# Kernel optimization log

Measured on AMD Instinct MI355X. Metric: run time of the kernel, lower is better.

Reference implementation:

```python
import jax, jax.numpy as jnp
import numpy as np

J = 17  # coco joints
SKEL = ((1, 2), (0, 1), (0, 2), (2, 4), (1, 3), (6, 8), (8, 10), (5, 7), (7, 9),
        (12, 14), (14, 16), (11, 13), (13, 15), (5, 6), (11, 12), (5, 11), (6, 12), (3, 5), (4, 6))
EPS = 1e-5


def make_adj():
    a = np.eye(J, dtype=np.float32)
    for i, j in SKEL:
        a[i, j] = 1.0
        a[j, i] = 1.0
    return jnp.asarray(a)


def conv_block(feat, W, b, g, be, adj):
    # feat: [B,V,Din], W: [V,Din,Dout], b/g/be: [V,Dout]
    h = jnp.einsum('bvd,vdo->bvo', feat, W) + b
    # BatchNorm1d (training mode): per-vertex, per-channel batch stats (biased var)
    mu = h.mean(axis=0)
    var = h.var(axis=0)
    h = (h - mu) * jax.lax.rsqrt(var + EPS) * g + be
    h = jnp.einsum('vu,buo->bvo', adj, h)  # adjacency aggregation
    return jax.nn.relu(h)


def setup_inputs() -> dict:
    key = jax.random.key(0)
    ks = jax.random.split(key, 10)
    B, Din = 8192, 2048
    s0 = 1.0 / np.sqrt(Din)
    s1 = 1.0 / np.sqrt(J)
    img_feat = jax.random.normal(ks[0], (B, J, Din), dtype=jnp.float32)
    # first GraphConvBlock: 2048 -> 17, per-vertex params
    W0 = jax.random.uniform(ks[1], (J, Din, J), jnp.float32, -s0, s0)
    b0 = jax.random.uniform(ks[2], (J, J), jnp.float32, -s0, s0)
    g0 = jnp.ones((J, J), jnp.float32)
    be0 = jnp.zeros((J, J), jnp.float32)
    # 4 GraphResBlocks x 2 GraphConvBlocks = 8 blocks of dim 17 -> 17
    Wr = jax.random.uniform(ks[3], (8, J, J, J), jnp.float32, -s1, s1)
    br = jax.random.uniform(ks[4], (8, J, J), jnp.float32, -s1, s1)
    gr = jnp.ones((8, J, J), jnp.float32)
    ber = jnp.zeros((8, J, J), jnp.float32)
    return {"img_feat": img_feat, "W0": W0, "b0": b0, "g0": g0, "be0": be0,
            "Wr": Wr, "br": br, "gr": gr, "ber": ber}


def reference(img_feat, W0, b0, g0, be0, Wr, br, gr, ber):
    adj = make_adj()
    feat = conv_block(img_feat, W0, b0, g0, be0, adj)  # [B,17,17]
    for r in range(4):  # 4 GraphResBlocks
        i0, i1 = 2 * r, 2 * r + 1
        h = conv_block(feat, Wr[i0], br[i0], gr[i0], ber[i0], adj)
        h = conv_block(h, Wr[i1], br[i1], gr[i1], ber[i1], adj)
        feat = h + feat  # residual
    return feat
```

## Files before the change

### kernel.cpp

```cpp
#include <hip/hip_runtime.h>

#define J 17
#define JP 18
#define VO 289
#define NB 8192
#define DIN 2048
#define EPSB 1e-5f
#define KC 512
#define RT 32
#define NCH 68

typedef __attribute__((ext_vector_type(8))) short bf16x8;
typedef __attribute__((ext_vector_type(4))) float f32x4;
typedef __attribute__((ext_vector_type(4))) float f32x4v;

__device__ __constant__ unsigned ADJM[J] = {
  0x7u, 0xFu, 0x17u, 0x2Au, 0x54u, 0x8E8u, 0x1170u, 0x2A0u, 0x540u,
  0x280u, 0x500u, 0x3820u, 0x5840u, 0xA800u, 0x15000u, 0xA000u, 0x14000u};

__device__ inline unsigned short f2bf(float x){
  unsigned u = __float_as_uint(x);
  return (unsigned short)((u + 0x7fffu + ((u>>16)&1u)) >> 16);
}

__global__ void zero_stats(float* p, int n) {
  int i = blockIdx.x*blockDim.x + threadIdx.x;
  int stride = gridDim.x*blockDim.x;
  for (; i < n; i += stride) p[i] = 0.f;
}

__global__ __launch_bounds__(256) void wconv_kernel(
    const float* __restrict__ W0, unsigned short* __restrict__ Wp)
{
  int t = blockIdx.x*256 + threadIdx.x;
  int v = t >> 11, k = t & 2047;
  const float* src = W0 + (size_t)t*J;
  unsigned short* dst = Wp + (((size_t)v*256 + (k>>3))*17)*8 + (k&7);
  #pragma unroll
  for (int o=0;o<J;++o)  dst[o*8] = f2bf(src[o]);
}

__global__ __launch_bounds__(256) void wfrag_kernel(
    const float* __restrict__ Wr, unsigned short* __restrict__ WfA,
    unsigned short* __restrict__ WfB)
{
  int t = blockIdx.x*256 + threadIdx.x;
  if (t < 8*17*64) {
    int s = t/(17*64), rem = t - s*17*64, v = rem>>6, ll = rem&63;
    int c = ll&15, o8 = ll>>4;
    unsigned short* dst = WfA + (size_t)t*8;
    const float* w = Wr + ((size_t)(s*J + v)*J)*J;
    #pragma unroll
    for (int j=0;j<8;++j){ int d=o8*8+j; dst[j] = (d<J) ? f2bf(w[(size_t)d*J + c]) : (unsigned short)0; }
  }
  if (t < 8*17*4) {
    int s = t/(17*4), rem = t - s*17*4, v = rem>>2, o8 = rem&3;
    unsigned short* dst = WfB + (size_t)t*8;
    const float* w = Wr + ((size_t)(s*J + v)*J)*J;
    #pragma unroll
    for (int j=0;j<8;++j){ int d=o8*8+j; dst[j] = (d<J) ? f2bf(w[(size_t)d*J + 16]) : (unsigned short)0; }
  }
}

__global__ __launch_bounds__(512) void conv0_kernel(
    const float* __restrict__ feat, const unsigned short* __restrict__ Wp,
    const float* __restrict__ b0, float* __restrict__ C,
    float* __restrict__ stat0)
{
  const int tid = threadIdx.x, w = tid>>6, l = tid&63;
  const int lo = l&15, oc = l>>4;
  const int sr = tid>>4, sc = tid&15;
  const int rowBase = blockIdx.x*RT;

  __shared__ __align__(16) unsigned short Ab[2][RT*KC];
  __shared__ float red[8][2][256];
  __shared__ float bS[VO], bQ[VO];

  for (int i=tid;i<VO;i+=512){ bS[i]=0.f; bQ[i]=0.f; }

  f32x4 acc00 = (f32x4){0.f,0.f,0.f,0.f};
  f32x4 acc01 = (f32x4){0.f,0.f,0.f,0.f};
  f32x4 acc10 = (f32x4){0.f,0.f,0.f,0.f};
  f32x4 acc11 = (f32x4){0.f,0.f,0.f,0.f};

  const float* frow = feat + (size_t)(rowBase + sr)*(J*DIN);
  f32x4v ld[8];

  auto issue = [&](int c){
    const f32x4v* src = (const f32x4v*)(frow + c*KC + sc*4);
    #pragma unroll
    for (int i=0;i<8;++i) ld[i] = __builtin_nontemporal_load(src + i*16);
  };
  auto writeLDS = [&](int buf){
    #pragma unroll
    for (int i=0;i<8;++i){
      ushort4 hv;
      hv.x=f2bf(ld[i].x); hv.y=f2bf(ld[i].y); hv.z=f2bf(ld[i].z); hv.w=f2bf(ld[i].w);
      const int f = sc*4 + i*64;
      *(ushort4*)&Ab[buf][(sr*KC + f) ^ ((sr&7)<<3)] = hv;
    }
  };

  issue(0); writeLDS(0);
  __syncthreads();

  const int swz = (lo&7)<<3;

  for (int c=0;c<NCH;++c){
    const int buf = c&1;
    if (c+1<NCH) issue(c+1);
    const int v = c>>2;
    #pragma unroll
    for (int ks=0;ks<2;++ks){
      const int kl = w*64 + ks*32 + oc*8;
      bf16x8 a0 = *(const bf16x8*)&Ab[buf][(lo*KC + kl) ^ swz];
      bf16x8 a1 = *(const bf16x8*)&Ab[buf][((16+lo)*KC + kl) ^ swz];
      const int kg8 = ((c&3)*KC + kl) >> 3;
      const unsigned short* fragBase = Wp + (((size_t)v*256 + kg8)*17)*8;
      bf16x8 bA = *(const bf16x8*)(fragBase + lo*8);
      bf16x8 bB = {0,0,0,0,0,0,0,0};
      if (lo==0) bB = *(const bf16x8*)(fragBase + 16*8);
      acc00 = __builtin_amdgcn_mfma_f32_16x16x32_bf16(a0, bA, acc00, 0,0,0);
      acc10 = __builtin_amdgcn_mfma_f32_16x16x32_bf16(a1, bA, acc10, 0,0,0);
      acc01 = __builtin_amdgcn_mfma_f32_16x16x32_bf16(a0, bB, acc01, 0,0,0);
      acc11 = __builtin_amdgcn_mfma_f32_16x16x32_bf16(a1, bB, acc11, 0,0,0);
    }
    if ((c&3)==3){
      #pragma unroll
      for (int pass=0; pass<2; ++pass){
        #pragma unroll
        for (int r=0;r<4;++r){
          red[w][0][(oc*4+r)*16+lo] = pass ? acc10[r] : acc00[r];
          red[w][1][(oc*4+r)*16+lo] = pass ? acc11[r] : acc01[r];
        }
        __syncthreads();
        if (tid < 256){
          const int er = tid>>4, ec = tid&15;
          const int ri = er*16+ec;
          float h0 = red[0][0][ri]+red[1][0][ri]+red[2][0][ri]+red[3][0][ri]
                   + red[4][0][ri]+red[5][0][ri]+red[6][0][ri]+red[7][0][ri]
                   + b0[v*J+ec];
          const int row = rowBase + pass*16 + er;
          C[(size_t)row*VO + v*J + ec] = h0;
          float s0 = h0, q0 = h0*h0;
          float s1 = 0.f, q1 = 0.f;
          if (ec==0){
            const int r2 = er*16;
            float h1 = red[0][1][r2]+red[1][1][r2]+red[2][1][r2]+red[3][1][r2]
                     + red[4][1][r2]+red[5][1][r2]+red[6][1][r2]+red[7][1][r2]
                     + b0[v*J+16];
            C[(size_t)row*VO + v*J + 16] = h1;
            s1 = h1; q1 = h1*h1;
          }
          s0 += __shfl_xor(s0,16); s0 += __shfl_xor(s0,32);
          q0 += __shfl_xor(q0,16); q0 += __shfl_xor(q0,32);
          s1 += __shfl_xor(s1,16); s1 += __shfl_xor(s1,32);
          q1 += __shfl_xor(q1,16); q1 += __shfl_xor(q1,32);
          if (l < 16){ atomicAdd(&bS[v*J+l], s0); atomicAdd(&bQ[v*J+l], q0); }
          if (l == 0){ atomicAdd(&bS[v*J+16], s1); atomicAdd(&bQ[v*J+16], q1); }
        }
        __syncthreads();
      }
      acc00 = (f32x4){0.f,0.f,0.f,0.f};
      acc01 = (f32x4){0.f,0.f,0.f,0.f};
      acc10 = (f32x4){0.f,0.f,0.f,0.f};
      acc11 = (f32x4){0.f,0.f,0.f,0.f};
    }
    if (c+1<NCH){
      writeLDS(buf^1);
      __syncthreads();
    }
  }

  __syncthreads();
  const int rep = blockIdx.x & 7;
  for (int i=tid;i<VO;i+=512){
    atomicAdd(&stat0[rep*512+i],        bS[i]);
    atomicAdd(&stat0[4096 + rep*512+i], bQ[i]);
  }
}

template<int RESID,int WRITEF,int CONV>
__global__ __launch_bounds__(256) void chain_kernel(
  const float* __restrict__ Cin, float* __restrict__ Cout,
  float* __restrict__ F,
  const float* __restrict__ statJ,
  const float* __restrict__ g, const float* __restrict__ be,
  const unsigned short* __restrict__ wfA_g, const unsigned short* __restrict__ wfB_g,
  const float* __restrict__ bc,
  float* __restrict__ statN)
{
  __shared__ float aC[VO], cC[VO], bb[VO];
  __shared__ float ssum[VO], ssq[VO];
  __shared__ float hb1[4][4][J*JP];
  __shared__ __align__(16) unsigned short hb2[16*576];

  const int tid = threadIdx.x, wv = tid>>6, lane = tid&63;
  const int lo = lane&15, oc = lane>>4;
  const int rowBase = blockIdx.x*16;

  for (int i=tid;i<VO;i+=256){
    float s=0.f,q=0.f;
    #pragma unroll
    for (int r=0;r<8;++r){ s += statJ[r*512+i]; q += statJ[4096 + r*512+i]; }
    float mu  = s*(1.f/NB);
    float var = q*(1.f/NB) - mu*mu;
    float A = rsqrtf(var + EPSB)*g[i];
    aC[i]=A; cC[i]=be[i]-mu*A;
    ssum[i]=0.f; ssq[i]=0.f;
    if (CONV) bb[i]=bc[i];
  }
  if (CONV){
    for (int i=tid;i<16*576/8;i+=256) ((uint4*)hb2)[i] = (uint4){0,0,0,0};
  }
  __syncthreads();

  #pragma unroll
  for (int r4=0;r4<4;++r4){
    const int row = wv*4 + r4;
    const float* cr = Cin + (size_t)(rowBase+row)*VO;
    #pragma unroll
    for (int s=0;s<5;++s){
      int vo = lane + 64*s;
      if (vo<VO){ int vtx=vo/J, o=vo-vtx*J; hb1[wv][r4][vtx*JP+o] = cr[vo]*aC[vo] + cC[vo]; }
    }
  }
  asm volatile("s_waitcnt lgkmcnt(0)" ::: "memory");
  #pragma unroll
  for (int r4=0;r4<4;++r4){
    const int row = wv*4 + r4;
    #pragma unroll
    for (int s=0;s<5;++s){
      int vo = lane + 64*s;
      if (vo<VO){
        int vtx=vo/J, o=vo-vtx*J;
        unsigned m = ADJM[vtx];
        float a = 0.f;
        while (m){ int u=__ffs(m)-1; m&=m-1; a += hb1[wv][r4][u*JP+o]; }
        a = a>0.f ? a : 0.f;
        size_t gi = (size_t)(rowBase+row)*VO + vo;
        if (RESID)  a += F[gi];
        if (WRITEF) F[gi] = a;
        if (CONV){
          int idx = (row*576 + vtx*32 + o) ^ ((row&7)<<3);
          hb2[idx] = f2bf(a);
        } else {
          Cout[gi] = a;
        }
      }
    }
  }
  if (!CONV) return;
  __syncthreads();

  for (int v=wv; v<J; v+=4){
    const int aidx = (lo*576 + v*32 + oc*8) ^ ((lo&7)<<3);
    bf16x8 a  = *(const bf16x8*)&hb2[aidx];
    bf16x8 bA = *(const bf16x8*)(wfA_g + ((size_t)v*64 + lane)*8);
    bf16x8 bB = {0,0,0,0,0,0,0,0};
    if (lo==0) bB = *(const bf16x8*)(wfB_g + ((size_t)v*4 + oc)*8);
    f32x4 acc0 = (f32x4){0.f,0.f,0.f,0.f};
    f32x4 acc1 = (f32x4){0.f,0.f,0.f,0.f};
    acc0 = __builtin_amdgcn_mfma_f32_16x16x32_bf16(a, bA, acc0, 0,0,0);
    acc1 = __builtin_amdgcn_mfma_f32_16x16x32_bf16(a, bB, acc1, 0,0,0);

    const float bias0 = bb[v*J+lo];
    const float bias1 = bb[v*J+16];
    float s0=0.f,q0=0.f,s1=0.f,q1=0.f;
    #pragma unroll
    for (int r=0;r<4;++r){
      const int row = rowBase + oc*4 + r;
      const float h0 = acc0[r] + bias0;
      Cout[(size_t)row*VO + v*J + lo] = h0;
      s0 += h0; q0 += h0*h0;
      if (lo==0){
        const float h1 = acc1[r] + bias1;
        Cout[(size_t)row*VO + v*J + 16] = h1;
        s1 += h1; q1 += h1*h1;
      }
    }
    s0 += __shfl_xor(s0,16); s0 += __shfl_xor(s0,32);
    q0 += __shfl_xor(q0,16); q0 += __shfl_xor(q0,32);
    s1 += __shfl_xor(s1,16); s1 += __shfl_xor(s1,32);
    q1 += __shfl_xor(q1,16); q1 += __shfl_xor(q1,32);
    if (lane < 16){ atomicAdd(&ssum[v*J+lo], s0); atomicAdd(&ssq[v*J+lo], q0); }
    if (lane == 0){ atomicAdd(&ssum[v*J+16], s1); atomicAdd(&ssq[v*J+16], q1); }
  }
  __syncthreads();
  const int rep = blockIdx.x & 7;
  for (int i=tid;i<VO;i+=256){
    atomicAdd(&statN[rep*512+i],        ssum[i]);
    atomicAdd(&statN[4096 + rep*512+i], ssq[i]);
  }
}

extern "C" void kernel_launch(void* const* d_in, const int* in_sizes, int n_in,
                              void* d_out, int out_size, void* d_ws, size_t ws_size,
                              hipStream_t stream)
{
  (void)in_sizes; (void)n_in; (void)out_size; (void)ws_size;
  const float* img = (const float*)d_in[0];
  const float* W0  = (const float*)d_in[1];
  const float* b0  = (const float*)d_in[2];
  const float* g0  = (const float*)d_in[3];
  const float* be0 = (const float*)d_in[4];
  const float* Wr  = (const float*)d_in[5];
  const float* br  = (const float*)d_in[6];
  const float* gr  = (const float*)d_in[7];
  const float* ber = (const float*)d_in[8];

  float* ws = (float*)d_ws;
  float* ST = ws;
  unsigned short* Wp  = (unsigned short*)(ws + 73728);
  unsigned short* WfA = (unsigned short*)(ws + 73728 + 300000);
  unsigned short* WfB = WfA + 8*17*64*8;
  float* Ca = ws + 73728 + 300000 + 40000;
  float* Cb = Ca + (size_t)NB*VO;
  float* F  = Cb + (size_t)NB*VO;
  float* out = (float*)d_out;

  zero_stats<<<72,256,0,stream>>>(ST, 9*8192);
  wconv_kernel<<<136,256,0,stream>>>(W0, Wp);
  wfrag_kernel<<<34,256,0,stream>>>(Wr, WfA, WfB);

  conv0_kernel<<<256,512,0,stream>>>(img, Wp, b0, Ca, ST);

  #define STG(j) (ST + (j)*8192)
  #define WFA(s) (WfA + (size_t)(s)*17*64*8)
  #define WFB(s) (WfB + (size_t)(s)*17*4*8)
  chain_kernel<0,1,1><<<512,256,0,stream>>>(Ca, Cb, F, STG(0), g0,      be0,
                                            WFA(0), WFB(0), br+0*VO, STG(1));
  chain_kernel<0,0,1><<<512,256,0,stream>>>(Cb, Ca, F, STG(1), gr+0*VO, ber+0*VO,
                                            WFA(1), WFB(1), br+1*VO, STG(2));
  chain_kernel<1,1,1><<<512,256,0,stream>>>(Ca, Cb, F, STG(2), gr+1*VO, ber+1*VO,
                                            WFA(2), WFB(2), br+2*VO, STG(3));
  chain_kernel<0,0,1><<<512,256,0,stream>>>(Cb, Ca, F, STG(3), gr+2*VO, ber+2*VO,
                                            WFA(3), WFB(3), br+3*VO, STG(4));
  chain_kernel<1,1,1><<<512,256,0,stream>>>(Ca, Cb, F, STG(4), gr+3*VO, ber+3*VO,
                                            WFA(4), WFB(4), br+4*VO, STG(5));
  chain_kernel<0,0,1><<<512,256,0,stream>>>(Cb, Ca, F, STG(5), gr+4*VO, ber+4*VO,
                                            WFA(5), WFB(5), br+5*VO, STG(6));
  chain_kernel<1,1,1><<<512,256,0,stream>>>(Ca, Cb, F, STG(6), gr+5*VO, ber+5*VO,
                                            WFA(6), WFB(6), br+6*VO, STG(7));
  chain_kernel<0,0,1><<<512,256,0,stream>>>(Cb, Ca, F, STG(7), gr+6*VO, ber+6*VO,
                                            WFA(7), WFB(7), br+7*VO, STG(8));
  chain_kernel<1,0,0><<<512,256,0,stream>>>(Ca, out, F, STG(8), gr+7*VO, ber+7*VO,
                                            nullptr, nullptr, nullptr, nullptr);
  #undef STG
  #undef WFA
  #undef WFB
}
```

Before: 408.6 us.

## Fuse nine chain launches into one cooperative persistent kernel with grid sync

Replaces the nine separate chain_kernel launches with a single cooperative kernel of 256 blocks that loops over the stages and uses grid.sync between them. Each block handles 32 rows per stage in two 16-row tiles, which removes per-launch overhead and kernel boundary gaps. The cost is 256 blocks instead of 512, so each block does more serial work and occupancy may be lower. It also adds grid-wide barrier latency. If the cooperative launch fails, the code falls back to the old multi-launch path.

New measurement: 950.6 us. 133% more time.

```diff
diff --git a/kernel.cpp b/kernel.cpp
--- a/kernel.cpp
+++ b/kernel.cpp
@@ -1,4 +1,6 @@
 #include <hip/hip_runtime.h>
+#include <hip/hip_cooperative_groups.h>
+namespace cg = cooperative_groups;
 
 #define J 17
 #define JP 18
@@ -294,6 +296,149 @@
   }
 }
 
+__global__ __launch_bounds__(256) void chainall_kernel(
+  float* __restrict__ Ca, float* __restrict__ Cb,
+  float* __restrict__ F, float* __restrict__ outF,
+  float* __restrict__ ST,
+  const float* __restrict__ g0, const float* __restrict__ be0,
+  const float* __restrict__ gr, const float* __restrict__ ber,
+  const unsigned short* __restrict__ WfA, const unsigned short* __restrict__ WfB,
+  const float* __restrict__ br)
+{
+  cg::grid_group grid = cg::this_grid();
+
+  __shared__ float aC[VO], cC[VO], bb[VO];
+  __shared__ float ssum[VO], ssq[VO];
+  __shared__ float hb1[4][4][J*JP];
+  __shared__ __align__(16) unsigned short hb2[16*576];
+
+  const int tid = threadIdx.x, wv = tid>>6, lane = tid&63;
+  const int lo = lane&15, oc = lane>>4;
+
+  for (int i=tid;i<16*576/8;i+=256) ((uint4*)hb2)[i] = (uint4){0,0,0,0};
+
+  for (int s=0; s<9; ++s){
+    const bool RESID  = (s==2||s==4||s==6||s==8);
+    const bool WRITEF = (s==0||s==2||s==4||s==6);
+    const bool CONV   = (s<8);
+    const float* Cin  = (s&1) ? Cb : Ca;
+    float*       Cout = (s==8) ? outF : ((s&1) ? Ca : Cb);
+    const float* statJ = ST + (size_t)s*8192;
+    float*       statN = ST + (size_t)(s+1)*8192;
+    const float* g_s  = (s==0) ? g0  : gr  + (size_t)(s-1)*VO;
+    const float* be_s = (s==0) ? be0 : ber + (size_t)(s-1)*VO;
+    const unsigned short* wfA_g = WfA + (size_t)s*17*64*8;
+    const unsigned short* wfB_g = WfB + (size_t)s*17*4*8;
+    const float* bc = br + (size_t)s*VO;
+
+    for (int i=tid;i<VO;i+=256){
+      float sm=0.f,q=0.f;
+      #pragma unroll
+      for (int r=0;r<8;++r){ sm += statJ[r*512+i]; q += statJ[4096 + r*512+i]; }
+      float mu  = sm*(1.f/NB);
+      float var = q*(1.f/NB) - mu*mu;
+      float A = rsqrtf(var + EPSB)*g_s[i];
+      aC[i]=A; cC[i]=be_s[i]-mu*A;
+      ssum[i]=0.f; ssq[i]=0.f;
+      if (CONV) bb[i]=bc[i];
+    }
+    __syncthreads();
+
+    for (int t=0;t<2;++t){
+      const int rowBase = blockIdx.x*32 + t*16;
+
+      #pragma unroll
+      for (int r4=0;r4<4;++r4){
+        const int row = wv*4 + r4;
+        const float* cr = Cin + (size_t)(rowBase+row)*VO;
+        #pragma unroll
+        for (int sl=0;sl<5;++sl){
+          int vo = lane + 64*sl;
+          if (vo<VO){ int vtx=vo/J, o=vo-vtx*J; hb1[wv][r4][vtx*JP+o] = cr[vo]*aC[vo] + cC[vo]; }
+        }
+      }
+      asm volatile("s_waitcnt lgkmcnt(0)" ::: "memory");
+      #pragma unroll
+      for (int r4=0;r4<4;++r4){
+        const int row = wv*4 + r4;
+        #pragma unroll
+        for (int sl=0;sl<5;++sl){
+          int vo = lane + 64*sl;
+          if (vo<VO){
+            int vtx=vo/J, o=vo-vtx*J;
+            unsigned m = ADJM[vtx];
+            float a = 0.f;
+            while (m){ int u=__ffs(m)-1; m&=m-1; a += hb1[wv][r4][u*JP+o]; }
+            a = a>0.f ? a : 0.f;
+            size_t gi = (size_t)(rowBase+row)*VO + vo;
+            if (RESID)  a += F[gi];
+            if (WRITEF) F[gi] = a;
+            if (CONV){
+              int idx = (row*576 + vtx*32 + o) ^ ((row&7)<<3);
+              hb2[idx] = f2bf(a);
+            } else {
+              Cout[gi] = a;
+            }
+          }
+        }
+      }
+
+      if (CONV){
+        __syncthreads();
+        for (int v=wv; v<J; v+=4){
+          const int aidx = (lo*576 + v*32 + oc*8) ^ ((lo&7)<<3);
+          bf16x8 a  = *(const bf16x8*)&hb2[aidx];
+          bf16x8 bA = *(const bf16x8*)(wfA_g + ((size_t)v*64 + lane)*8);
+          bf16x8 bB = {0,0,0,0,0,0,0,0};
+          if (lo==0) bB = *(const bf16x8*)(wfB_g + ((size_t)v*4 + oc)*8);
+          f32x4 acc0 = (f32x4){0.f,0.f,0.f,0.f};
+          f32x4 acc1 = (f32x4){0.f,0.f,0.f,0.f};
+          acc0 = __builtin_amdgcn_mfma_f32_16x16x32_bf16(a, bA, acc0, 0,0,0);
+          acc1 = __builtin_amdgcn_mfma_f32_16x16x32_bf16(a, bB, acc1, 0,0,0);
+
+          const float bias0 = bb[v*J+lo];
+          const float bias1 = bb[v*J+16];
+          float s0=0.f,q0=0.f,s1=0.f,q1=0.f;
+          #pragma unroll
+          for (int r=0;r<4;++r){
+            const int row = rowBase + oc*4 + r;
+            const float h0 = acc0[r] + bias0;
+            Cout[(size_t)row*VO + v*J + lo] = h0;
+            s0 += h0; q0 += h0*h0;
+            if (lo==0){
+              const float h1 = acc1[r] + bias1;
+              Cout[(size_t)row*VO + v*J + 16] = h1;
+              s1 += h1; q1 += h1*h1;
+            }
+          }
+          s0 += __shfl_xor(s0,16); s0 += __shfl_xor(s0,32);
+          q0 += __shfl_xor(q0,16); q0 += __shfl_xor(q0,32);
+          s1 += __shfl_xor(s1,16); s1 += __shfl_xor(s1,32);
+          q1 += __shfl_xor(q1,16); q1 += __shfl_xor(q1,32);
+          if (lane < 16){ atomicAdd(&ssum[v*J+lo], s0); atomicAdd(&ssq[v*J+lo], q0); }
+          if (lane == 0){ atomicAdd(&ssum[v*J+16], s1); atomicAdd(&ssq[v*J+16], q1); }
+        }
+        __syncthreads();
+      } else {
+        __syncthreads();
+      }
+    }
+
+    if (CONV){
+      const int rep = blockIdx.x & 7;
+      for (int i=tid;i<VO;i+=256){
+        atomicAdd(&statN[rep*512+i],        ssum[i]);
+        atomicAdd(&statN[4096 + rep*512+i], ssq[i]);
+      }
+    }
+
+    if (s<8){
+      __threadfence();
+      grid.sync();
+    }
+  }
+}
+
 extern "C" void kernel_launch(void* const* d_in, const int* in_sizes, int n_in,
                               void* d_out, int out_size, void* d_ws, size_t ws_size,
                               hipStream_t stream)
@@ -325,28 +470,35 @@
 
   conv0_kernel<<<256,512,0,stream>>>(img, Wp, b0, Ca, ST);
 
-  #define STG(j) (ST + (j)*8192)
-  #define WFA(s) (WfA + (size_t)(s)*17*64*8)
-  #define WFB(s) (WfB + (size_t)(s)*17*4*8)
-  chain_kernel<0,1,1><<<512,256,0,stream>>>(Ca, Cb, F, STG(0), g0,      be0,
-                                            WFA(0), WFB(0), br+0*VO, STG(1));
-  chain_kernel<0,0,1><<<512,256,0,stream>>>(Cb, Ca, F, STG(1), gr+0*VO, ber+0*VO,
-                                            WFA(1), WFB(1), br+1*VO, STG(2));
-  chain_kernel<1,1,1><<<512,256,0,stream>>>(Ca, Cb, F, STG(2), gr+1*VO, ber+1*VO,
-                                            WFA(2), WFB(2), br+2*VO, STG(3));
-  chain_kernel<0,0,1><<<512,256,0,stream>>>(Cb, Ca, F, STG(3), gr+2*VO, ber+2*VO,
-                                            WFA(3), WFB(3), br+3*VO, STG(4));
-  chain_kernel<1,1,1><<<512,256,0,stream>>>(Ca, Cb, F, STG(4), gr+3*VO, ber+3*VO,
-                                            WFA(4), WFB(4), br+4*VO, STG(5));
-  chain_kernel<0,0,1><<<512,256,0,stream>>>(Cb, Ca, F, STG(5), gr+4*VO, ber+4*VO,
-                                            WFA(5), WFB(5), br+5*VO, STG(6));
-  chain_kernel<1,1,1><<<512,256,0,stream>>>(Ca, Cb, F, STG(6), gr+5*VO, ber+5*VO,
-                                            WFA(6), WFB(6), br+6*VO, STG(7));
-  chain_kernel<0,0,1><<<512,256,0,stream>>>(Cb, Ca, F, STG(7), gr+6*VO, ber+6*VO,
-                                            WFA(7), WFB(7), br+7*VO, STG(8));
-  chain_kernel<1,0,0><<<512,256,0,stream>>>(Ca, out, F, STG(8), gr+7*VO, ber+7*VO,
-                                            nullptr, nullptr, nullptr, nullptr);
-  #undef STG
-  #undef WFA
-  #undef WFB
-}
+  void* args[] = { (void*)&Ca, (void*)&Cb, (void*)&F, (void*)&out, (void*)&ST,
+                   (void*)&g0, (void*)&be0, (void*)&gr, (void*)&ber,
+                   (void*)&WfA, (void*)&WfB, (void*)&br };
+  hipError_t cerr = hipLaunchCooperativeKernel((const void*)chainall_kernel,
+                                               dim3(256), dim3(256), args, 0, stream);
+  if (cerr != hipSuccess) {
+    #define STG(j) (ST + (j)*8192)
+    #define WFA(s) (WfA + (size_t)(s)*17*64*8)
+    #define WFB(s) (WfB + (size_t)(s)*17*4*8)
+    chain_kernel<0,1,1><<<512,256,0,stream>>>(Ca, Cb, F, STG(0), g0,      be0,
+                                              WFA(0), WFB(0), br+0*VO, STG(1));
+    chain_kernel<0,0,1><<<512,256,0,stream>>>(Cb, Ca, F, STG(1), gr+0*VO, ber+0*VO,
+                                              WFA(1), WFB(1), br+1*VO, STG(2));
+    chain_kernel<1,1,1><<<512,256,0,stream>>>(Ca, Cb, F, STG(2), gr+1*VO, ber+1*VO,
+                                              WFA(2), WFB(2), br+2*VO, STG(3));
+    chain_kernel<0,0,1><<<512,256,0,stream>>>(Cb, Ca, F, STG(3), gr+2*VO, ber+2*VO,
+                                              WFA(3), WFB(3), br+3*VO, STG(4));
+    chain_kernel<1,1,1><<<512,256,0,stream>>>(Ca, Cb, F, STG(4), gr+3*VO, ber+3*VO,
+                                              WFA(4), WFB(4), br+4*VO, STG(5));
+    chain_kernel<0,0,1><<<512,256,0,stream>>>(Cb, Ca, F, STG(5), gr+4*VO, ber+4*VO,
+                                              WFA(5), WFB(5), br+5*VO, STG(6));
+    chain_kernel<1,1,1><<<512,256,0,stream>>>(Ca, Cb, F, STG(6), gr+5*VO, ber+5*VO,
+                                              WFA(6), WFB(6), br+6*VO, STG(7));
+    chain_kernel<0,0,1><<<512,256,0,stream>>>(Cb, Ca, F, STG(7), gr+6*VO, ber+6*VO,
+                                              WFA(7), WFB(7), br+7*VO, STG(8));
+    chain_kernel<1,0,0><<<512,256,0,stream>>>(Ca, out, F, STG(8), gr+7*VO, ber+7*VO,
+                                              nullptr, nullptr, nullptr, nullptr);
+    #undef STG
+    #undef WFA
+    #undef WFB
+  }
+}
```
